# Kernel tuning notes

Measured on AMD Instinct MI355X. Metric: run time of the kernel, lower is better.

## Reference

```python
import jax, jax.numpy as jnp
import numpy as np

B, N, F_IN, F_OUT = 8, 2048, 64, 64
NEG = -9.0e15  # matches torch's -9000000000000000.0 mask value


def setup_inputs() -> dict:
    key = jax.random.key(0)
    ks = jax.random.split(key, 12)
    stdv1 = 1.0 / np.sqrt(F_IN)
    stdv2 = 1.0 / np.sqrt(2 * F_OUT)
    x = jax.random.normal(ks[0], (B, N, F_IN), dtype=jnp.float32)
    adj = jax.random.randint(ks[1], (B, N, N), 0, 2).astype(jnp.int32)
    identity = jnp.broadcast_to(jnp.eye(N, dtype=jnp.int32), (B, N, N))
    def unif(k, shape, s):
        return jax.random.uniform(k, shape, jnp.float32, -s, s)
    return {
        "x": x, "adj": adj, "identity": identity,
        "W1": unif(ks[2], (F_OUT, F_IN), stdv1), "b1": unif(ks[3], (F_OUT,), stdv1),
        "a1": unif(ks[4], (1, 2 * F_OUT), stdv2), "ab1": unif(ks[5], (1,), stdv2),
        "W2": unif(ks[6], (F_OUT, F_IN), stdv1), "b2": unif(ks[7], (F_OUT,), stdv1),
        "a2": unif(ks[8], (1, 2 * F_OUT), stdv2), "ab2": unif(ks[9], (1,), stdv2),
    }


def _gat_layer(x, mask, W, b, a, ab):
    # linear1
    h = jnp.einsum('bnf,of->bno', x, W) + b                     # [B,N,Fo]
    Fo = h.shape[-1]
    # linear2 on concat(h_i, h_j) decomposes: e_ij = relu(h_i.a1 + h_j.a2 + ab)
    s1 = h @ a[0, :Fo]                                          # [B,N]
    s2 = h @ a[0, Fo:]                                          # [B,N]
    e = jax.nn.relu(s1[:, :, None] + s2[:, None, :] + ab[0])    # [B,N,N]
    e = jnp.where(mask > 0, e, NEG)
    att = jax.nn.softmax(e, axis=2)                             # [B,N,N]
    return jnp.einsum('bnm,bmf->bnf', att, h)                   # dropout p=0 / eval


def reference(x, adj, identity, W1, b1, a1, ab1, W2, b2, a2, ab2):
    out1 = _gat_layer(x, adj, W1, b1, a1, ab1)
    out2 = _gat_layer(x, identity, W2, b2, a2, ab2)
    return out1 + out2
```

## Files before the change

kernel.cpp:

```cpp
#include <hip/hip_runtime.h>


#define DEVI __device__ __forceinline__

typedef __attribute__((ext_vector_type(8))) short short8;
typedef __attribute__((ext_vector_type(4))) float floatx4;

DEVI unsigned short f2bf(float x) {
    unsigned u = __builtin_bit_cast(unsigned, x);
    unsigned r = u + 0x7FFFu + ((u >> 16) & 1u);
    return (unsigned short)(r >> 16);
}

DEVI short8 pack8(const float* v) {
    short8 r;
#pragma unroll
    for (int i = 0; i < 8; ++i) r[i] = (short)f2bf(v[i]);
    return r;
}

DEVI unsigned cvt_pk_bf16(float lo, float hi) {
    unsigned r;
    asm("v_cvt_pk_bf16_f32 %0, %1, %2" : "=v"(r) : "v"(lo), "v"(hi));
    return r;
}

DEVI void team_sync() {
    __builtin_amdgcn_sched_barrier(0);
    asm volatile("s_waitcnt lgkmcnt(0)" ::: "memory");
    __builtin_amdgcn_s_barrier();
    __builtin_amdgcn_sched_barrier(0);
}

__global__ __launch_bounds__(256) void k_prep(
    const float* __restrict__ x, const float* __restrict__ W1,
    const float* __restrict__ b1, const float* __restrict__ a1,
    const float* __restrict__ ab1,
    unsigned short* __restrict__ hT1,
    float* __restrict__ expt1,
    float* __restrict__ expv)
{
    __shared__ __align__(16) unsigned short hstage[64][72];
    const int tid = threadIdx.x;
    const int w = tid >> 6, lane = tid & 63;
    const int g = lane >> 4, r15 = lane & 15;
    const int blockRow = blockIdx.x * 64;
    const int rowbase = blockRow + w * 16;

    float xa[8], xb[8];
    const float* xrow = x + (long)(rowbase + r15) * 64;
#pragma unroll
    for (int e = 0; e < 8; ++e) { xa[e] = xrow[g * 8 + e]; xb[e] = xrow[32 + g * 8 + e]; }
    short8 A0 = pack8(xa), A1 = pack8(xb);

    floatx4 acc[4];
#pragma unroll
    for (int nt = 0; nt < 4; ++nt) {
        float wa[8], wb[8];
        const float* wrow = W1 + (nt * 16 + r15) * 64;
#pragma unroll
        for (int e = 0; e < 8; ++e) { wa[e] = wrow[g * 8 + e]; wb[e] = wrow[32 + g * 8 + e]; }
        short8 B0 = pack8(wa), B1 = pack8(wb);
        floatx4 c = {0.f, 0.f, 0.f, 0.f};
        c = __builtin_amdgcn_mfma_f32_16x16x32_bf16(A0, B0, c, 0, 0, 0);
        c = __builtin_amdgcn_mfma_f32_16x16x32_bf16(A1, B1, c, 0, 0, 0);
        float bias = b1[nt * 16 + r15];
#pragma unroll
        for (int q = 0; q < 4; ++q) c[q] += bias;
        acc[nt] = c;
    }

    float a1lo[4], a1hi[4];
#pragma unroll
    for (int nt = 0; nt < 4; ++nt) {
        a1lo[nt] = a1[nt * 16 + r15];
        a1hi[nt] = a1[64 + nt * 16 + r15];
    }
    float s1q[4], s2q[4];
#pragma unroll
    for (int q = 0; q < 4; ++q) {
        float s1 = 0.f, s2 = 0.f;
#pragma unroll
        for (int nt = 0; nt < 4; ++nt) { s1 += acc[nt][q] * a1lo[nt]; s2 += acc[nt][q] * a1hi[nt]; }
#pragma unroll
        for (int m = 1; m < 16; m <<= 1) { s1 += __shfl_xor(s1, m); s2 += __shfl_xor(s2, m); }
        s1q[q] = s1; s2q[q] = s2;
    }
    if (r15 == 0) {
        float abv = ab1[0];
#pragma unroll
        for (int q = 0; q < 4; ++q) {
            expt1[rowbase + 4 * g + q] = __expf(s1q[q] + abv);
            expv[rowbase + 4 * g + q]  = __expf(s2q[q]);
        }
    }

#pragma unroll
    for (int nt = 0; nt < 4; ++nt)
#pragma unroll
        for (int q = 0; q < 4; ++q)
            hstage[nt * 16 + r15][w * 16 + 4 * g + q] = f2bf(acc[nt][q]);
    __syncthreads();
    {
        const int o = tid >> 2, seg = (tid & 3) * 16;
        const int bb = blockRow >> 11;
        const int ib = blockRow & 2047;
        unsigned short* dst = hT1 + ((long)(bb * 64 + o) * 2048) + ib + seg;
        uint4 v0 = *(const uint4*)&hstage[o][seg];
        uint4 v1 = *(const uint4*)&hstage[o][seg + 8];
        *(uint4*)dst = v0;
        *(uint4*)(dst + 8) = v1;
    }
}

__global__ __launch_bounds__(512, 4) void k_attn(
    const float* __restrict__ x, const int* __restrict__ adj,
    const float* __restrict__ W2, const float* __restrict__ b2,
    const unsigned short* __restrict__ hT1,
    const float* __restrict__ expt1, const float* __restrict__ expv,
    float* __restrict__ out)
{
    __shared__ __align__(16) unsigned short hl[4][2][64][64];
    __shared__ __align__(16) float vlds[2048];

    const int tid = threadIdx.x;
    const int w = tid >> 6, lane = tid & 63;
    const int t = w >> 1, wrow = w & 1;
    const int g = lane >> 4, r15 = lane & 15;
    const int bb = blockIdx.x & 7;
    const int it = blockIdx.x >> 3;
    const int rowbase = it * 32 + wrow * 16;
    const int jt0 = t * 8;

    *(float4*)&vlds[tid * 4] = *(const float4*)&expv[bb * 2048 + tid * 4];

    const float u = expt1[bb * 2048 + rowbase + r15];

    floatx4 acc[4];
#pragma unroll
    for (int nt = 0; nt < 4; ++nt) acc[nt] = (floatx4){0.f, 0.f, 0.f, 0.f};
    floatx4 acc5 = {0.f, 0.f, 0.f, 0.f};

    short8 ones;
#pragma unroll
    for (int i = 0; i < 8; ++i) ones[i] = (short)0x3F80;

    const int4* adjq = (const int4*)(adj + (long)(bb * 2048 + rowbase + r15) * 2048);

    const int ttid = tid & 127;
    const int so = ttid >> 1, ch = ttid & 1;
    const unsigned short* hTsrc = hT1 + (long)(bb * 64 + so) * 2048 + ch * 32;
    unsigned short* hlw = &hl[t][0][0][0];

    int4 adjR[2][4];
    uint4 hrg[4];

#define ADJ(c) do {                                                            \
        const int base_ = (jt0 + (c)) * 16 + g * 2;                            \
        adjR[(c) & 1][0] = adjq[base_];                                        \
        adjR[(c) & 1][1] = adjq[base_ + 1];                                    \
        adjR[(c) & 1][2] = adjq[base_ + 8];                                    \
        adjR[(c) & 1][3] = adjq[base_ + 9];                                    \
    } while (0)

#define HTLOAD(c) do {                                                         \
        const unsigned short* s_ = hTsrc + (jt0 + (c)) * 64;                   \
        hrg[0] = *(const uint4*)s_;                                            \
        hrg[1] = *(const uint4*)(s_ + 8);                                      \
        hrg[2] = *(const uint4*)(s_ + 16);                                     \
        hrg[3] = *(const uint4*)(s_ + 24);                                     \
    } while (0)

#define HTSTORE(c) do {                                                        \
        const int bo_ = ((c) & 1) * 4096 + so * 64;                            \
        _Pragma("unroll")                                                      \
        for (int k_ = 0; k_ < 4; ++k_)                                         \
            *(uint4*)&hlw[bo_ + (((ch * 4 + k_) ^ (so & 7)) * 8)] = hrg[k_];   \
    } while (0)

#define COMPUTE(C) do {                                                        \
        const int vb_ = (jt0 + (C)) * 64 + g * 8;                              \
        float4 v0_ = *(const float4*)&vlds[vb_];                               \
        float4 v1_ = *(const float4*)&vlds[vb_ + 4];                           \
        float4 v2_ = *(const float4*)&vlds[vb_ + 32];                          \
        float4 v3_ = *(const float4*)&vlds[vb_ + 36];                          \
        int4 j0_ = adjR[(C) & 1][0], j1_ = adjR[(C) & 1][1];                   \
        int4 j2_ = adjR[(C) & 1][2], j3_ = adjR[(C) & 1][3];                   \
        uint4 au_, bu_;                                                        \
        au_.x = cvt_pk_bf16(j0_.x > 0 ? fmaxf(u * v0_.x, 1.f) : 0.f,           \
                            j0_.y > 0 ? fmaxf(u * v0_.y, 1.f) : 0.f);          \
        au_.y = cvt_pk_bf16(j0_.z > 0 ? fmaxf(u * v0_.z, 1.f) : 0.f,           \
                            j0_.w > 0 ? fmaxf(u * v0_.w, 1.f) : 0.f);          \
        au_.z = cvt_pk_bf16(j1_.x > 0 ? fmaxf(u * v1_.x, 1.f) : 0.f,           \
                            j1_.y > 0 ? fmaxf(u * v1_.y, 1.f) : 0.f);          \
        au_.w = cvt_pk_bf16(j1_.z > 0 ? fmaxf(u * v1_.z, 1.f) : 0.f,           \
                            j1_.w > 0 ? fmaxf(u * v1_.w, 1.f) : 0.f);          \
        bu_.x = cvt_pk_bf16(j2_.x > 0 ? fmaxf(u * v2_.x, 1.f) : 0.f,           \
                            j2_.y > 0 ? fmaxf(u * v2_.y, 1.f) : 0.f);          \
        bu_.y = cvt_pk_bf16(j2_.z > 0 ? fmaxf(u * v2_.z, 1.f) : 0.f,           \
                            j2_.w > 0 ? fmaxf(u * v2_.w, 1.f) : 0.f);          \
        bu_.z = cvt_pk_bf16(j3_.x > 0 ? fmaxf(u * v3_.x, 1.f) : 0.f,           \
                            j3_.y > 0 ? fmaxf(u * v3_.y, 1.f) : 0.f);          \
        bu_.w = cvt_pk_bf16(j3_.z > 0 ? fmaxf(u * v3_.z, 1.f) : 0.f,           \
                            j3_.w > 0 ? fmaxf(u * v3_.w, 1.f) : 0.f);          \
        short8 a0 = __builtin_bit_cast(short8, au_);                           \
        short8 a1 = __builtin_bit_cast(short8, bu_);                           \
        const int bufo_ = ((C) & 1) * 4096;                                    \
        const int sw_ = r15 & 7;                                               \
        _Pragma("unroll")                                                      \
        for (int nt_ = 0; nt_ < 4; ++nt_) {                                    \
            const int ro_ = bufo_ + (nt_ * 16 + r15) * 64;                     \
            short8 b0 = *(const short8*)&hlw[ro_ + ((g ^ sw_) * 8)];           \
            short8 b1 = *(const short8*)&hlw[ro_ + (((4 + g) ^ sw_) * 8)];     \
            acc[nt_] = __builtin_amdgcn_mfma_f32_16x16x32_bf16(a0, b0, acc[nt_], 0, 0, 0); \
            acc[nt_] = __builtin_amdgcn_mfma_f32_16x16x32_bf16(a1, b1, acc[nt_], 0, 0, 0); \
        }                                                                      \
        acc5 = __builtin_amdgcn_mfma_f32_16x16x32_bf16(a0, ones, acc5, 0, 0, 0); \
        acc5 = __builtin_amdgcn_mfma_f32_16x16x32_bf16(a1, ones, acc5, 0, 0, 0); \
    } while (0)

    ADJ(0); ADJ(1);
    HTLOAD(0);
    HTSTORE(0);
    team_sync();

#pragma unroll
    for (int C = 0; C < 8; ++C) {
        if (C < 7) HTLOAD(C + 1);
        COMPUTE(C);
        if (C < 7) HTSTORE(C + 1);
        if (C < 6) ADJ(C + 2);
        team_sync();
    }

#undef COMPUTE
#undef HTSTORE
#undef HTLOAD
#undef ADJ

    float* csh = (float*)&hl[0][0][0][0];
    if (t > 0) {
        const int wb = ((t - 1) * 2 + wrow) * 20;
#pragma unroll
        for (int nt = 0; nt < 4; ++nt)
#pragma unroll
            for (int q = 0; q < 4; ++q)
                csh[(wb + nt * 4 + q) * 64 + lane] = acc[nt][q];
#pragma unroll
        for (int q = 0; q < 4; ++q)
            csh[(wb + 16 + q) * 64 + lane] = acc5[q];
    }
    __syncthreads();

    if (t == 0) {
#pragma unroll
        for (int ti = 0; ti < 3; ++ti) {
            const int wb = (ti * 2 + wrow) * 20;
#pragma unroll
            for (int nt = 0; nt < 4; ++nt)
#pragma unroll
                for (int q = 0; q < 4; ++q)
                    acc[nt][q] += csh[(wb + nt * 4 + q) * 64 + lane];
#pragma unroll
            for (int q = 0; q < 4; ++q)
                acc5[q] += csh[(wb + 16 + q) * 64 + lane];
        }
        float linv[4];
#pragma unroll
        for (int q = 0; q < 4; ++q) linv[q] = 1.0f / acc5[q];

        float xa[8], xb[8];
        const float* xrow = x + ((long)(bb * 2048 + rowbase + r15)) * 64;
#pragma unroll
        for (int e = 0; e < 8; ++e) { xa[e] = xrow[g * 8 + e]; xb[e] = xrow[32 + g * 8 + e]; }
        short8 A0 = pack8(xa), A1 = pack8(xb);
#pragma unroll
        for (int nt = 0; nt < 4; ++nt) {
            float wa[8], wb[8];
            const float* wrow2 = W2 + (nt * 16 + r15) * 64;
#pragma unroll
            for (int e = 0; e < 8; ++e) { wa[e] = wrow2[g * 8 + e]; wb[e] = wrow2[32 + g * 8 + e]; }
            short8 B0 = pack8(wa), B1 = pack8(wb);
            floatx4 c = {0.f, 0.f, 0.f, 0.f};
            c = __builtin_amdgcn_mfma_f32_16x16x32_bf16(A0, B0, c, 0, 0, 0);
            c = __builtin_amdgcn_mfma_f32_16x16x32_bf16(A1, B1, c, 0, 0, 0);
            float bias = b2[nt * 16 + r15];
#pragma unroll
            for (int q = 0; q < 4; ++q) {
                float val = acc[nt][q] * linv[q] + c[q] + bias;
                out[((long)(bb * 2048 + rowbase + 4 * g + q)) * 64 + nt * 16 + r15] = val;
            }
        }
    }
}

extern "C" void kernel_launch(void* const* d_in, const int* in_sizes, int n_in,
                              void* d_out, int out_size, void* d_ws, size_t ws_size,
                              hipStream_t stream) {
    const float* x   = (const float*)d_in[0];
    const int*   adj = (const int*)d_in[1];
    const float* W1  = (const float*)d_in[3];
    const float* b1  = (const float*)d_in[4];
    const float* a1  = (const float*)d_in[5];
    const float* ab1 = (const float*)d_in[6];
    const float* W2  = (const float*)d_in[7];
    const float* b2  = (const float*)d_in[8];

    unsigned short* hT1 = (unsigned short*)d_ws;
    float* expt1 = (float*)((char*)d_ws + (size_t)8 * 64 * 2048 * 2);
    float* expv  = expt1 + 8 * 2048;

    k_prep<<<256, 256, 0, stream>>>(x, W1, b1, a1, ab1, hT1, expt1, expv);
    k_attn<<<512, 512, 0, stream>>>(x, adj, W2, b2, hT1, expt1, expv, (float*)d_out);
}
```

Before: 40.33 us.

## Preload adjacency tile as ballot bitmasks in LDS, read expv from global

```diff
diff --git a/kernel.cpp b/kernel.cpp
--- a/kernel.cpp
+++ b/kernel.cpp
@@ -5,6 +5,7 @@
 
 typedef __attribute__((ext_vector_type(8))) short short8;
 typedef __attribute__((ext_vector_type(4))) float floatx4;
+typedef unsigned long long ull;
 
 DEVI unsigned short f2bf(float x) {
     unsigned u = __builtin_bit_cast(unsigned, x);
@@ -121,7 +122,7 @@
     float* __restrict__ out)
 {
     __shared__ __align__(16) unsigned short hl[4][2][64][64];
-    __shared__ __align__(16) float vlds[2048];
+    __shared__ __align__(16) ull msk[32][32];
 
     const int tid = threadIdx.x;
     const int w = tid >> 6, lane = tid & 63;
@@ -132,9 +133,31 @@
     const int rowbase = it * 32 + wrow * 16;
     const int jt0 = t * 8;
 
-    *(float4*)&vlds[tid * 4] = *(const float4*)&expv[bb * 2048 + tid * 4];
+    {
+        const int* arow = adj + (long)(bb * 2048 + it * 32 + w * 4) * 2048 + lane;
+#pragma unroll 2
+        for (int rr = 0; rr < 4; ++rr) {
+            const int* r_ = arow + (long)rr * 2048;
+#pragma unroll
+            for (int cc = 0; cc < 8; ++cc) {
+                int a0 = r_[cc * 256];
+                int a1 = r_[cc * 256 + 64];
+                int a2 = r_[cc * 256 + 128];
+                int a3 = r_[cc * 256 + 192];
+                ull b0 = __ballot(a0 > 0);
+                ull b1 = __ballot(a1 > 0);
+                ull b2v = __ballot(a2 > 0);
+                ull b3 = __ballot(a3 > 0);
+                if (lane < 4) {
+                    ull b = lane == 0 ? b0 : lane == 1 ? b1 : lane == 2 ? b2v : b3;
+                    msk[cc * 4 + lane][w * 4 + rr] = b;
+                }
+            }
+        }
+    }
 
     const float u = expt1[bb * 2048 + rowbase + r15];
+    const float* expvb = expv + bb * 2048;
 
     floatx4 acc[4];
 #pragma unroll
@@ -144,24 +167,13 @@
     short8 ones;
 #pragma unroll
     for (int i = 0; i < 8; ++i) ones[i] = (short)0x3F80;
-
-    const int4* adjq = (const int4*)(adj + (long)(bb * 2048 + rowbase + r15) * 2048);
 
     const int ttid = tid & 127;
     const int so = ttid >> 1, ch = ttid & 1;
     const unsigned short* hTsrc = hT1 + (long)(bb * 64 + so) * 2048 + ch * 32;
     unsigned short* hlw = &hl[t][0][0][0];
 
-    int4 adjR[2][4];
     uint4 hrg[4];
-
-#define ADJ(c) do {                                                            \
-        const int base_ = (jt0 + (c)) * 16 + g * 2;                            \
-        adjR[(c) & 1][0] = adjq[base_];                                        \
-        adjR[(c) & 1][1] = adjq[base_ + 1];                                    \
-        adjR[(c) & 1][2] = adjq[base_ + 8];                                    \
-        adjR[(c) & 1][3] = adjq[base_ + 9];                                    \
-    } while (0)
 
 #define HTLOAD(c) do {                                                         \
         const unsigned short* s_ = hTsrc + (jt0 + (c)) * 64;                   \
@@ -178,31 +190,26 @@
             *(uint4*)&hlw[bo_ + (((ch * 4 + k_) ^ (so & 7)) * 8)] = hrg[k_];   \
     } while (0)
 
+#define PX(mm, bit, val) (((mm) & (1u << (bit))) ? fmaxf(u * (val), 1.f) : 0.f)
+
 #define COMPUTE(C) do {                                                        \
         const int vb_ = (jt0 + (C)) * 64 + g * 8;                              \
-        float4 v0_ = *(const float4*)&vlds[vb_];                               \
-        float4 v1_ = *(const float4*)&vlds[vb_ + 4];                           \
-        float4 v2_ = *(const float4*)&vlds[vb_ + 32];                          \
-        float4 v3_ = *(const float4*)&vlds[vb_ + 36];                          \
-        int4 j0_ = adjR[(C) & 1][0], j1_ = adjR[(C) & 1][1];                   \
-        int4 j2_ = adjR[(C) & 1][2], j3_ = adjR[(C) & 1][3];                   \
+        float4 v0_ = *(const float4*)&expvb[vb_];                              \
+        float4 v1_ = *(const float4*)&expvb[vb_ + 4];                          \
+        float4 v2_ = *(const float4*)&expvb[vb_ + 32];                         \
+        float4 v3_ = *(const float4*)&expvb[vb_ + 36];                         \
+        ull m64_ = msk[jt0 + (C)][wrow * 16 + r15];                            \
+        unsigned m0_ = ((unsigned)m64_ >> (g * 8)) & 0xFFu;                    \
+        unsigned m1_ = ((unsigned)(m64_ >> 32) >> (g * 8)) & 0xFFu;            \
         uint4 au_, bu_;                                                        \
-        au_.x = cvt_pk_bf16(j0_.x > 0 ? fmaxf(u * v0_.x, 1.f) : 0.f,           \
-                            j0_.y > 0 ? fmaxf(u * v0_.y, 1.f) : 0.f);          \
-        au_.y = cvt_pk_bf16(j0_.z > 0 ? fmaxf(u * v0_.z, 1.f) : 0.f,           \
-                            j0_.w > 0 ? fmaxf(u * v0_.w, 1.f) : 0.f);          \
-        au_.z = cvt_pk_bf16(j1_.x > 0 ? fmaxf(u * v1_.x, 1.f) : 0.f,           \
-                            j1_.y > 0 ? fmaxf(u * v1_.y, 1.f) : 0.f);          \
-        au_.w = cvt_pk_bf16(j1_.z > 0 ? fmaxf(u * v1_.z, 1.f) : 0.f,           \
-                            j1_.w > 0 ? fmaxf(u * v1_.w, 1.f) : 0.f);          \
-        bu_.x = cvt_pk_bf16(j2_.x > 0 ? fmaxf(u * v2_.x, 1.f) : 0.f,           \
-                            j2_.y > 0 ? fmaxf(u * v2_.y, 1.f) : 0.f);          \
-        bu_.y = cvt_pk_bf16(j2_.z > 0 ? fmaxf(u * v2_.z, 1.f) : 0.f,           \
-                            j2_.w > 0 ? fmaxf(u * v2_.w, 1.f) : 0.f);          \
-        bu_.z = cvt_pk_bf16(j3_.x > 0 ? fmaxf(u * v3_.x, 1.f) : 0.f,           \
-                            j3_.y > 0 ? fmaxf(u * v3_.y, 1.f) : 0.f);          \
-        bu_.w = cvt_pk_bf16(j3_.z > 0 ? fmaxf(u * v3_.z, 1.f) : 0.f,           \
-                            j3_.w > 0 ? fmaxf(u * v3_.w, 1.f) : 0.f);          \
+        au_.x = cvt_pk_bf16(PX(m0_, 0, v0_.x), PX(m0_, 1, v0_.y));             \
+        au_.y = cvt_pk_bf16(PX(m0_, 2, v0_.z), PX(m0_, 3, v0_.w));             \
+        au_.z = cvt_pk_bf16(PX(m0_, 4, v1_.x), PX(m0_, 5, v1_.y));             \
+        au_.w = cvt_pk_bf16(PX(m0_, 6, v1_.z), PX(m0_, 7, v1_.w));             \
+        bu_.x = cvt_pk_bf16(PX(m1_, 0, v2_.x), PX(m1_, 1, v2_.y));             \
+        bu_.y = cvt_pk_bf16(PX(m1_, 2, v2_.z), PX(m1_, 3, v2_.w));             \
+        bu_.z = cvt_pk_bf16(PX(m1_, 4, v3_.x), PX(m1_, 5, v3_.y));             \
+        bu_.w = cvt_pk_bf16(PX(m1_, 6, v3_.z), PX(m1_, 7, v3_.w));             \
         short8 a0 = __builtin_bit_cast(short8, au_);                           \
         short8 a1 = __builtin_bit_cast(short8, bu_);                           \
         const int bufo_ = ((C) & 1) * 4096;                                    \
@@ -219,8 +226,8 @@
         acc5 = __builtin_amdgcn_mfma_f32_16x16x32_bf16(a1, ones, acc5, 0, 0, 0); \
     } while (0)
 
-    ADJ(0); ADJ(1);
     HTLOAD(0);
+    __syncthreads();
     HTSTORE(0);
     team_sync();
 
@@ -229,14 +236,13 @@
         if (C < 7) HTLOAD(C + 1);
         COMPUTE(C);
         if (C < 7) HTSTORE(C + 1);
-        if (C < 6) ADJ(C + 2);
         team_sync();
     }
 
 #undef COMPUTE
+#undef PX
 #undef HTSTORE
 #undef HTLOAD
-#undef ADJ
 
     float* csh = (float*)&hl[0][0][0][0];
     if (t > 0) {
```

Result: slower. 60.83 us (+50.8%).
